# Kernel tuning notes

Hardware: AMD Instinct MI355X
Metric: run time of the kernel (lower is better)

## Reference

```python
import jax, jax.numpy as jnp
import numpy as np

B, I, D = 512, 128, 64


def setup_inputs() -> dict:
    key = jax.random.key(0)
    embeddings = jax.random.normal(key, (B, I, D), dtype=jnp.float32)
    return {"embeddings": embeddings}


def reference(embeddings):
    # Original: em_ij[b,i,j,d] = emb[b,i,d]*emb[b,j,d]; ctx = mean over j.
    # Algebraically: ctx[b,i,d] = emb[b,i,d] * mean_j emb[b,j,d] -- linear time,
    # no [B,I,I,D] materialization.
    mean_emb = jnp.mean(embeddings, axis=1, keepdims=True)  # [B,1,D]
    ctx_vec = embeddings * mean_emb                         # [B,I,D]
    # activation_function (undefined in the snippet; repo uses a smooth
    # pointwise activation -- tanh assumed). Dropout is identity in eval mode.
    return jnp.tanh(ctx_vec)
```

## Files before the change

### kernel.cpp

```cpp
#include <hip/hip_runtime.h>


#define BB 512
#define II 128
#define DD 64
#define ELEMS_PER_BATCH (II * DD)
#define VEC_PER_BATCH   (ELEMS_PER_BATCH / 4)
#define BLOCK 512
#define VPT   (VEC_PER_BATCH / BLOCK)
#define WAVES (BLOCK / 64)

typedef float f4 __attribute__((ext_vector_type(4)));

__device__ __forceinline__ float fast_tanh(float x) {
    float e = __expf(2.0f * x);
    return __fmaf_rn(-2.0f, __builtin_amdgcn_rcpf(e + 1.0f), 1.0f);
}

__global__ __launch_bounds__(BLOCK, 4) void ctx_tanh_kernel(
        const float* __restrict__ emb, float* __restrict__ out) {
    __shared__ f4 s_part[WAVES * 16];
    __shared__ f4 s_mean[16];

    const int b = blockIdx.x;
    const int t = threadIdx.x;
    const f4* __restrict__ gin  = (const f4*)(emb + (size_t)b * ELEMS_PER_BATCH);
    f4* __restrict__       gout = (f4*)(out + (size_t)b * ELEMS_PER_BATCH);

    f4 v[VPT];
    #pragma unroll
    for (int k = 0; k < VPT; ++k) v[k] = gin[t + BLOCK * k];

    f4 acc = v[0];
    #pragma unroll
    for (int k = 1; k < VPT; ++k) acc += v[k];

    acc.x += __shfl_xor(acc.x, 16); acc.y += __shfl_xor(acc.y, 16);
    acc.z += __shfl_xor(acc.z, 16); acc.w += __shfl_xor(acc.w, 16);
    acc.x += __shfl_xor(acc.x, 32); acc.y += __shfl_xor(acc.y, 32);
    acc.z += __shfl_xor(acc.z, 32); acc.w += __shfl_xor(acc.w, 32);

    const int lane = t & 63;
    const int wave = t >> 6;
    if (lane < 16) s_part[wave * 16 + lane] = acc;
    __syncthreads();

    if (t < 16) {
        f4 s = s_part[t];
        #pragma unroll
        for (int w = 1; w < WAVES; ++w) s += s_part[w * 16 + t];
        s *= (1.0f / (float)II);
        s_mean[t] = s;
    }
    __syncthreads();

    const f4 m4 = s_mean[t & 15];
    #pragma unroll
    for (int k = 0; k < VPT; ++k) {
        f4 o;
        o.x = fast_tanh(v[k].x * m4.x);
        o.y = fast_tanh(v[k].y * m4.y);
        o.z = fast_tanh(v[k].z * m4.z);
        o.w = fast_tanh(v[k].w * m4.w);
        __builtin_nontemporal_store(o, &gout[t + BLOCK * k]);
    }
}

extern "C" void kernel_launch(void* const* d_in, const int* in_sizes, int n_in,
                              void* d_out, int out_size, void* d_ws, size_t ws_size,
                              hipStream_t stream) {
    const float* emb = (const float*)d_in[0];
    float* out = (float*)d_out;
    ctx_tanh_kernel<<<dim3(BB), dim3(BLOCK), 0, stream>>>(emb, out);
}
```

Before: 66.14 us.

## Split fused mean-and-tanh kernel into separate mean and apply kernels

```diff
diff --git a/kernel.cpp b/kernel.cpp
--- a/kernel.cpp
+++ b/kernel.cpp
@@ -6,9 +6,7 @@
 #define DD 64
 #define ELEMS_PER_BATCH (II * DD)
 #define VEC_PER_BATCH   (ELEMS_PER_BATCH / 4)
-#define BLOCK 512
-#define VPT   (VEC_PER_BATCH / BLOCK)
-#define WAVES (BLOCK / 64)
+#define MEAN_VECS       (DD / 4)
 
 typedef float f4 __attribute__((ext_vector_type(4)));
 
@@ -17,52 +15,70 @@
     return __fmaf_rn(-2.0f, __builtin_amdgcn_rcpf(e + 1.0f), 1.0f);
 }
 
-__global__ __launch_bounds__(BLOCK, 4) void ctx_tanh_kernel(
-        const float* __restrict__ emb, float* __restrict__ out) {
-    __shared__ f4 s_part[WAVES * 16];
-    __shared__ f4 s_mean[16];
+#define BLK_A 256
+#define VPT_A (VEC_PER_BATCH / BLK_A)
+
+__global__ __launch_bounds__(BLK_A) void mean_kernel(
+        const float* __restrict__ emb, float* __restrict__ means) {
+    __shared__ f4 s_part[4 * 16];
 
     const int b = blockIdx.x;
     const int t = threadIdx.x;
-    const f4* __restrict__ gin  = (const f4*)(emb + (size_t)b * ELEMS_PER_BATCH);
-    f4* __restrict__       gout = (f4*)(out + (size_t)b * ELEMS_PER_BATCH);
+    const f4* __restrict__ gin = (const f4*)(emb + (size_t)b * ELEMS_PER_BATCH);
 
-    f4 v[VPT];
+    f4 v[VPT_A];
     #pragma unroll
-    for (int k = 0; k < VPT; ++k) v[k] = gin[t + BLOCK * k];
-
+    for (int k = 0; k < VPT_A; ++k) v[k] = gin[t + BLK_A * k];
     f4 acc = v[0];
     #pragma unroll
-    for (int k = 1; k < VPT; ++k) acc += v[k];
+    for (int k = 1; k < VPT_A; ++k) acc += v[k];
 
     acc.x += __shfl_xor(acc.x, 16); acc.y += __shfl_xor(acc.y, 16);
     acc.z += __shfl_xor(acc.z, 16); acc.w += __shfl_xor(acc.w, 16);
     acc.x += __shfl_xor(acc.x, 32); acc.y += __shfl_xor(acc.y, 32);
     acc.z += __shfl_xor(acc.z, 32); acc.w += __shfl_xor(acc.w, 32);
 
-    const int lane = t & 63;
-    const int wave = t >> 6;
+    const int lane = t & 63, wave = t >> 6;
     if (lane < 16) s_part[wave * 16 + lane] = acc;
     __syncthreads();
 
     if (t < 16) {
-        f4 s = s_part[t];
-        #pragma unroll
-        for (int w = 1; w < WAVES; ++w) s += s_part[w * 16 + t];
+        f4 s = s_part[t] + s_part[16 + t] + s_part[32 + t] + s_part[48 + t];
         s *= (1.0f / (float)II);
-        s_mean[t] = s;
+        ((f4*)means)[(size_t)b * MEAN_VECS + t] = s;
     }
-    __syncthreads();
+}
 
-    const f4 m4 = s_mean[t & 15];
+#define BLK_B 256
+#define GRID_B 2048
+#define TOTAL_VECS (BB * VEC_PER_BATCH)
+#define VPT_B (TOTAL_VECS / (GRID_B * BLK_B))
+
+__global__ __launch_bounds__(BLK_B) void apply_kernel(
+        const float* __restrict__ emb, const float* __restrict__ means,
+        float* __restrict__ out) {
+    const f4* __restrict__ gin  = (const f4*)emb;
+    const f4* __restrict__ gm   = (const f4*)means;
+    f4* __restrict__       gout = (f4*)out;
+
+    const int base = blockIdx.x * BLK_B + threadIdx.x;
+
+    f4 x[VPT_B], m[VPT_B];
     #pragma unroll
-    for (int k = 0; k < VPT; ++k) {
+    for (int k = 0; k < VPT_B; ++k) {
+        const int v = base + k * (GRID_B * BLK_B);
+        x[k] = gin[v];
+        m[k] = gm[(size_t)(v >> 11) * MEAN_VECS + (v & 15)];
+    }
+    #pragma unroll
+    for (int k = 0; k < VPT_B; ++k) {
+        const int v = base + k * (GRID_B * BLK_B);
         f4 o;
-        o.x = fast_tanh(v[k].x * m4.x);
-        o.y = fast_tanh(v[k].y * m4.y);
-        o.z = fast_tanh(v[k].z * m4.z);
-        o.w = fast_tanh(v[k].w * m4.w);
-        __builtin_nontemporal_store(o, &gout[t + BLOCK * k]);
+        o.x = fast_tanh(x[k].x * m[k].x);
+        o.y = fast_tanh(x[k].y * m[k].y);
+        o.z = fast_tanh(x[k].z * m[k].z);
+        o.w = fast_tanh(x[k].w * m[k].w);
+        __builtin_nontemporal_store(o, &gout[v]);
     }
 }
 
@@ -71,5 +87,8 @@
                               hipStream_t stream) {
     const float* emb = (const float*)d_in[0];
     float* out = (float*)d_out;
-    ctx_tanh_kernel<<<dim3(BB), dim3(BLOCK), 0, stream>>>(emb, out);
+    float* means = (float*)d_ws;
+
+    mean_kernel<<<dim3(BB), dim3(BLK_A), 0, stream>>>(emb, means);
+    apply_kernel<<<dim3(GRID_B), dim3(BLK_B), 0, stream>>>(emb, means, out);
 }
```

Result: slower. 71.75 us (+8.5%).
